# Kernel tuning notes

Measured on AMD Instinct MI355X. Metric: run time of the kernel, lower is better.

The kernel has to match this reference:

```python
import jax, jax.numpy as jnp
import numpy as np

# Geometry / physics constants (match init_kwargs)
NS = 128
NX = 512
NY = 512
NT = 2048
DT = 4e-08          # grid.dt [s]
C = 1500.0          # speed of sound [m/s]
T0 = 0.0            # sensor_array.t0
T_MAX = (NT - 2) * DT  # grid.t_max, chosen so d0+1 stays in-bounds after clamp


def setup_inputs() -> dict:
    key = jax.random.key(0)
    kx, = jax.random.split(key, 1)
    # recorded pressure signals: (1, Ns, Nt)
    x = jax.random.normal(kx, (1, NS, NT), dtype=jnp.float32)
    # sensors on a ring of radius 5 cm centered on the imaging region
    ang = jnp.arange(NS, dtype=jnp.float32) * (2.0 * np.pi / NS)
    sensors = jnp.stack([0.02 + 0.05 * jnp.cos(ang),
                         0.02 + 0.05 * jnp.sin(ang)], axis=-1)  # (Ns, 2)
    # pixel grid covering a 4x4 cm region -> (Nx*Ny, 2)
    xs = jnp.linspace(0.0, 0.04, NX, dtype=jnp.float32)
    ys = jnp.linspace(0.0, 0.04, NY, dtype=jnp.float32)
    gx, gy = jnp.meshgrid(xs, ys, indexing='ij')
    grid_pts = jnp.stack([gx.ravel(), gy.ravel()], axis=-1)  # (Nx*Ny, 2)
    return {"x": x, "sensors": sensors, "grid_pts": grid_pts}


def reference(x, sensors, grid_pts):
    # delay-and-sum (linear interp), fully vectorized over sensors and pixels.
    # distance: (Ns, P) with P = Nx*Ny
    diff = grid_pts[None, :, :] - sensors[:, None, :]
    distance = jnp.sqrt(jnp.sum(diff * diff, axis=-1))
    idx = (distance / C + T0) / DT                      # fractional time index
    idx = jnp.where((idx > T_MAX / DT) | (idx < 0.0), 0.0, idx)
    d0 = jnp.floor(idx)
    w0 = idx - d0          # NOTE: original applies w0 to the floor sample
    w1 = 1.0 - w0          # (d1 - idx), applied to the ceil sample
    i0 = d0.astype(jnp.int32)
    sig = x[0]                                          # (Ns, Nt)
    y0 = jnp.take_along_axis(sig, i0, axis=1)           # (Ns, P)
    y1 = jnp.take_along_axis(sig, i0 + 1, axis=1)       # (Ns, P)
    img = jnp.sum(w0 * y0 + w1 * y1, axis=0)            # (P,)
    return img.reshape(1, NX, NY)
```

## Files before the change

### kernel.cpp

```cpp
#include <hip/hip_runtime.h>

#define NS 128
#define NX 512
#define NY 512
#define NT 2048
#define WIN 64
#define TI 16
#define TJ 16


__device__ __forceinline__ float sqrt_cr(float x) {
    const float r0 = __builtin_amdgcn_sqrtf(x);
    const float rd = __int_as_float(__float_as_int(r0) - 1);
    const float ru = __int_as_float(__float_as_int(r0) + 1);
    const float vd = fmaf(-rd, r0, x);
    const float vu = fmaf(-ru, r0, x);
    float r = (vd <= 0.0f) ? rd : r0;
    r = (vu > 0.0f) ? ru : r;
    return r;
}

__global__ __launch_bounds__(512, 8) void das_kernel(
        const float* __restrict__ x,
        const float* __restrict__ sensors,
        const float* __restrict__ grid,
        float* __restrict__ out) {
    __shared__ float4 rec[NS];
    __shared__ float win[NS * WIN];
    __shared__ float part[2][512];

    const int tid = threadIdx.x;
    const int bi = blockIdx.x;
    const int ti = bi >> 5;
    const int tj = bi & 31;

    if (tid < NS) {
        const float2 sv = reinterpret_cast<const float2*>(sensors)[tid];
        const float2 gc = reinterpret_cast<const float2*>(
            grid)[(ti * TI + 8) * NY + (tj * TJ + 8)];
        const float dx = gc.x - sv.x;
        const float dy = gc.y - sv.y;
        const float idxc = __builtin_amdgcn_sqrtf(dx * dx + dy * dy)
                           * (1.0f / 1500.0f) * (1.0f / 4e-08f);
        const int ws = (int)idxc - 31;
        rec[tid] = make_float4(sv.x, sv.y,
                               __int_as_float(tid * WIN - ws),
                               __int_as_float(tid * NT + ws));
    }
    __syncthreads();

    const int wv = tid >> 6;
    const int lane = tid & 63;
#pragma unroll
    for (int r = 0; r < NS / 8; ++r) {
        const int s = r * 8 + wv;
        const int gb = __float_as_int(rec[s].w);
        win[s * WIN + lane] = x[gb + lane];
    }
    __syncthreads();

    const int quad = tid >> 7;
    const int pl = tid & 127;
    const int p0 = (ti * TI + (pl >> 4)) * NY + (tj * TJ + (pl & 15));
    const int p1 = p0 + 8 * NY;

    const float2 g0 = reinterpret_cast<const float2*>(grid)[p0];
    const float2 g1 = reinterpret_cast<const float2*>(grid)[p1];

    const float inv_c = 1.0f / 1500.0f;
    const float inv_dt = 1.0f / 4e-08f;

    const int sbase = __builtin_amdgcn_readfirstlane(quad << 5);
    const float4* recp = rec + sbase;

    float accA0 = 0.0f, accB0 = 0.0f;
    float accA1 = 0.0f, accB1 = 0.0f;
#pragma unroll
    for (int s = 0; s < 32; ++s) {
        const float4 rc = recp[s];
        const float svx = rc.x;
        const float svy = rc.y;
        const int o = __float_as_int(rc.z);

        const float dx0 = g0.x - svx;
        const float dy0 = g0.y - svy;
        const float dist0 = sqrt_cr(dx0 * dx0 + dy0 * dy0);
        const float idx0 = dist0 * inv_c * inv_dt;
        const int i00 = (int)idx0;
        const float w00 = __builtin_amdgcn_fractf(idx0);

        const float dx1 = g1.x - svx;
        const float dy1 = g1.y - svy;
        const float dist1 = sqrt_cr(dx1 * dx1 + dy1 * dy1);
        const float idx1 = dist1 * inv_c * inv_dt;
        const int i10 = (int)idx1;
        const float w10 = __builtin_amdgcn_fractf(idx1);

        const float* wp0 = &win[i00 + o];
        const float* wp1 = &win[i10 + o];
        const float y00 = wp0[0];
        const float y01 = wp0[1];
        const float y10 = wp1[0];
        const float y11 = wp1[1];

        accA0 = fmaf(w00, y00 - y01, accA0);  accB0 += y01;
        accA1 = fmaf(w10, y10 - y11, accA1);  accB1 += y11;
    }

    part[0][tid] = accA0 + accB0;
    part[1][tid] = accA1 + accB1;
    __syncthreads();
    if (tid < 256) {
        const int t = tid;
        const int c = t >> 7;
        const int q = t & 127;
        const float v = part[c][q] + part[c][q + 128]
                      + part[c][q + 256] + part[c][q + 384];
        out[(ti * TI + (t >> 4)) * NY + (tj * TJ + (t & 15))] = v;
    }
}

extern "C" void kernel_launch(void* const* d_in, const int* in_sizes, int n_in,
                              void* d_out, int out_size, void* d_ws, size_t ws_size,
                              hipStream_t stream) {
    const float* x = (const float*)d_in[0];
    const float* sensors = (const float*)d_in[1];
    const float* grid = (const float*)d_in[2];
    float* out = (float*)d_out;

    const int nblocks = (NX / TI) * (NY / TJ);
    das_kernel<<<nblocks, 512, 0, stream>>>(x, sensors, grid, out);
}
```

Baseline: 24.57 us.

## Give each wave 16 sensors and 4 pixels per lane instead of 32 sensors and 2 pixels

Reassigns work so each of the 8 waves handles 16 sensors for 4 pixels per lane (64 pixels per wave), rather than 4 sensor-groups of 32 over 2 pixels. Each sensor record read from LDS is reused across four pixels, and the unrolled loop exposes more independent sqrt and LDS gathers for latency hiding. In exchange the cross-wave reduction now sums 8 partials in two rounds with extra barriers, and register pressure rises with four pixel accumulator pairs.

Result: slower. 71.86 us (+192.4%).

```diff
diff --git a/kernel.cpp b/kernel.cpp
--- a/kernel.cpp
+++ b/kernel.cpp
@@ -59,24 +59,25 @@
     }
     __syncthreads();
 
-    const int quad = tid >> 7;
-    const int pl = tid & 127;
-    const int p0 = (ti * TI + (pl >> 4)) * NY + (tj * TJ + (pl & 15));
-    const int p1 = p0 + 8 * NY;
+    const int col = tj * TJ + (lane & 15);
+    const int row0 = ti * TI + (lane >> 4);
+    const int pbase = row0 * NY + col;
 
-    const float2 g0 = reinterpret_cast<const float2*>(grid)[p0];
-    const float2 g1 = reinterpret_cast<const float2*>(grid)[p1];
+    const float2 g0 = reinterpret_cast<const float2*>(grid)[pbase];
+    const float2 g1 = reinterpret_cast<const float2*>(grid)[pbase + 4 * NY];
+    const float2 g2 = reinterpret_cast<const float2*>(grid)[pbase + 8 * NY];
+    const float2 g3 = reinterpret_cast<const float2*>(grid)[pbase + 12 * NY];
 
     const float inv_c = 1.0f / 1500.0f;
     const float inv_dt = 1.0f / 4e-08f;
 
-    const int sbase = __builtin_amdgcn_readfirstlane(quad << 5);
+    const int sbase = __builtin_amdgcn_readfirstlane(wv << 4);
     const float4* recp = rec + sbase;
 
-    float accA0 = 0.0f, accB0 = 0.0f;
-    float accA1 = 0.0f, accB1 = 0.0f;
+    float aA0 = 0.0f, aB0 = 0.0f, aA1 = 0.0f, aB1 = 0.0f;
+    float aA2 = 0.0f, aB2 = 0.0f, aA3 = 0.0f, aB3 = 0.0f;
 #pragma unroll
-    for (int s = 0; s < 32; ++s) {
+    for (int s = 0; s < 16; ++s) {
         const float4 rc = recp[s];
         const float svx = rc.x;
         const float svy = rc.y;
@@ -88,35 +89,57 @@
         const float idx0 = dist0 * inv_c * inv_dt;
         const int i00 = (int)idx0;
         const float w00 = __builtin_amdgcn_fractf(idx0);
-
         const float dx1 = g1.x - svx;
         const float dy1 = g1.y - svy;
         const float dist1 = sqrt_cr(dx1 * dx1 + dy1 * dy1);
         const float idx1 = dist1 * inv_c * inv_dt;
         const int i10 = (int)idx1;
         const float w10 = __builtin_amdgcn_fractf(idx1);
+        const float dx2 = g2.x - svx;
+        const float dy2 = g2.y - svy;
+        const float dist2 = sqrt_cr(dx2 * dx2 + dy2 * dy2);
+        const float idx2 = dist2 * inv_c * inv_dt;
+        const int i20 = (int)idx2;
+        const float w20 = __builtin_amdgcn_fractf(idx2);
+        const float dx3 = g3.x - svx;
+        const float dy3 = g3.y - svy;
+        const float dist3 = sqrt_cr(dx3 * dx3 + dy3 * dy3);
+        const float idx3 = dist3 * inv_c * inv_dt;
+        const int i30 = (int)idx3;
+        const float w30 = __builtin_amdgcn_fractf(idx3);
 
         const float* wp0 = &win[i00 + o];
         const float* wp1 = &win[i10 + o];
-        const float y00 = wp0[0];
-        const float y01 = wp0[1];
-        const float y10 = wp1[0];
-        const float y11 = wp1[1];
+        const float* wp2 = &win[i20 + o];
+        const float* wp3 = &win[i30 + o];
+        const float y00 = wp0[0], y01 = wp0[1];
+        const float y10 = wp1[0], y11 = wp1[1];
+        const float y20 = wp2[0], y21 = wp2[1];
+        const float y30 = wp3[0], y31 = wp3[1];
 
-        accA0 = fmaf(w00, y00 - y01, accA0);  accB0 += y01;
-        accA1 = fmaf(w10, y10 - y11, accA1);  accB1 += y11;
+        aA0 = fmaf(w00, y00 - y01, aA0);  aB0 += y01;
+        aA1 = fmaf(w10, y10 - y11, aA1);  aB1 += y11;
+        aA2 = fmaf(w20, y20 - y21, aA2);  aB2 += y21;
+        aA3 = fmaf(w30, y30 - y31, aA3);  aB3 += y31;
     }
 
-    part[0][tid] = accA0 + accB0;
-    part[1][tid] = accA1 + accB1;
-    __syncthreads();
-    if (tid < 256) {
-        const int t = tid;
-        const int c = t >> 7;
-        const int q = t & 127;
-        const float v = part[c][q] + part[c][q + 128]
-                      + part[c][q + 256] + part[c][q + 384];
-        out[(ti * TI + (t >> 4)) * NY + (tj * TJ + (t & 15))] = v;
+    const float a0 = aA0 + aB0, a1 = aA1 + aB1;
+    const float a2 = aA2 + aB2, a3 = aA3 + aB3;
+#pragma unroll
+    for (int r = 0; r < 2; ++r) {
+        part[0][tid] = (r == 0) ? a0 : a2;
+        part[1][tid] = (r == 0) ? a1 : a3;
+        __syncthreads();
+        if (tid < 128) {
+            const int kl = tid >> 6;
+            const int l = tid & 63;
+            float v = part[kl][l];
+#pragma unroll
+            for (int w = 1; w < 8; ++w) v += part[kl][w * 64 + l];
+            const int row = ti * TI + (l >> 4) + 4 * (2 * r + kl);
+            out[row * NY + (tj * TJ + (l & 15))] = v;
+        }
+        __syncthreads();
     }
 }
 
```
